# Optimization experiments

Hardware: AMD Instinct MI355X
Metric: run time of the kernel (lower is better)

Reference implementation:

```python
import jax, jax.numpy as jnp
import numpy as np

H, W, WS = 48, 48, 8          # spatial grid and window radius
D, NUM_HEADS = 256, 8          # embed dim, heads
N = H * W
K = (2 * WS + 1) ** 2          # max neighbors = 289
EPS = 1e-5


def _precompute_neighbors(h, w, ws):
    """Faithful port of SCAM._precompute_neighbors (pads ragged rows with n[0])."""
    neighbors_list = []
    for idx in range(h * w):
        row, col = idx // w, idx % w
        nb = []
        for i in range(-ws, ws + 1):
            for j in range(-ws, ws + 1):
                r, c = row + i, col + j
                if 0 <= r < h and 0 <= c < w:
                    nb.append(r * w + c)
        neighbors_list.append(nb)
    max_n = max(len(n) for n in neighbors_list)
    padded = np.array([n + [n[0]] * (max_n - len(n)) for n in neighbors_list], dtype=np.int32)
    return padded


def setup_inputs() -> dict:
    key = jax.random.key(0)
    k1, k2, k3, k4 = jax.random.split(key, 4)
    B = 1
    scale = 0.02
    return {
        "x1": jax.random.normal(k1, (B, N, D), dtype=jnp.float32),
        "x2": jax.random.normal(k2, (B, N, D), dtype=jnp.float32),
        "ln_gamma": jnp.ones((D,), jnp.float32),
        "ln_beta": jnp.zeros((D,), jnp.float32),
        "in_proj_w": jax.random.normal(k3, (3 * D, D), dtype=jnp.float32) * scale,
        "in_proj_b": jnp.zeros((3 * D,), jnp.float32),
        "out_w": jax.random.normal(k4, (D, D), dtype=jnp.float32) * scale,
        "out_b": jnp.zeros((D,), jnp.float32),
        "neighbors_idx": jnp.asarray(_precompute_neighbors(H, W, WS)),  # [N, K] int32
    }


def _layernorm(x, gamma, beta):
    mu = jnp.mean(x, axis=-1, keepdims=True)
    var = jnp.var(x, axis=-1, keepdims=True)
    return (x - mu) * jax.lax.rsqrt(var + EPS) * gamma + beta


def reference(x1, x2, ln_gamma, ln_beta, in_proj_w, in_proj_b, out_w, out_b, neighbors_idx):
    B, n, d = x1.shape
    hd = d // NUM_HEADS

    # --- neighborhood gather-attention on x2 ---
    neighbor_feats = x2[:, neighbors_idx, :]                         # [B, N, K, D]
    scores = jnp.einsum('bnd,bnkd->bnk', x2, neighbor_feats) / (d ** 0.5)
    attn_w = jax.nn.softmax(scores, axis=-1)                          # softmax over neighbors
    x2_fused = jnp.einsum('bnk,bnkd->bnd', attn_w, neighbor_feats)    # [B, N, D]
    x2_fused = _layernorm(x2_fused, ln_gamma, ln_beta)

    # --- standard MHA: query=x2_fused, key=value=x1 ---
    wq, wk, wv = in_proj_w[:d], in_proj_w[d:2 * d], in_proj_w[2 * d:]
    bq, bk, bv = in_proj_b[:d], in_proj_b[d:2 * d], in_proj_b[2 * d:]
    q = (x2_fused @ wq.T + bq).reshape(B, n, NUM_HEADS, hd).transpose(0, 2, 1, 3)
    k = (x1 @ wk.T + bk).reshape(B, n, NUM_HEADS, hd).transpose(0, 2, 1, 3)
    v = (x1 @ wv.T + bv).reshape(B, n, NUM_HEADS, hd).transpose(0, 2, 1, 3)
    logits = jnp.einsum('bhqd,bhkd->bhqk', q, k) / (hd ** 0.5)        # [B, H, N, N]
    p = jax.nn.softmax(logits, axis=-1)
    o = jnp.einsum('bhqk,bhkd->bhqd', p, v)                           # [B, H, N, hd]
    o = o.transpose(0, 2, 1, 3).reshape(B, n, d)
    return o @ out_w.T + out_b
```

## Files before the change

### kernel.cpp

```cpp
#include <hip/hip_runtime.h>
#include <math.h>

#define N 2304
#define D 256
#define K_NB 289
#define NH 8
#define HD 32
#define KS 4
#define SEG (N / KS)
#define NGR 2320

typedef __attribute__((ext_vector_type(8))) short short8;
typedef __attribute__((ext_vector_type(4))) float floatx4;

static __device__ __forceinline__ unsigned short f2bf(float x) {
  union { float f; unsigned u; } v; v.f = x;
  unsigned r = (v.u + 0x7fffu + ((v.u >> 16) & 1u)) >> 16;
  return (unsigned short)r;
}

__global__ __launch_bounds__(256) void prep_kernel(
    const float* __restrict__ x2, unsigned short* __restrict__ x2b_full,
    unsigned short* __restrict__ x2t_full)
{
  __shared__ unsigned short T[16][17];
  const int tx = threadIdx.x & 15;
  const int ty = threadIdx.x >> 4;
  const int k0 = blockIdx.x * 16;
  const int f0 = blockIdx.y * 16;
  const int key = k0 + ty - 8;
  unsigned short v = 0;
  if (key >= 0 && key < N) v = f2bf(x2[(size_t)key * D + f0 + tx]);
  x2b_full[(size_t)(k0 + ty) * D + f0 + tx] = v;
  T[ty][tx] = v;
  __syncthreads();
  x2t_full[(size_t)(f0 + ty) * NGR + k0 + tx] = T[tx][ty];
}

__global__ __launch_bounds__(256) void stage1_mfma_kernel(
    const unsigned short* __restrict__ x2b,
    const unsigned short* __restrict__ x2t,
    const float* __restrict__ gamma, const float* __restrict__ beta,
    float* __restrict__ x2f)
{
  __shared__ float S[16][548];
  __shared__ __align__(16) unsigned short Pb[16][552];
  __shared__ float dinv[16];
  __shared__ float lr1[4][16], lr2[4][16];

  const int t    = threadIdx.x;
  const int w    = t >> 6;
  const int lane = t & 63;
  const int g    = lane >> 4;
  const int cL   = lane & 15;
  const int b  = blockIdx.x;
  const int r  = b / 3;
  const int c0 = (b % 3) * 16;
  const int qbase = r * 48 + c0;
  const int row_lo = max(0, 8 - r);
  const int row_hi = min(16, 55 - r);

  short8 qf[8];
  {
    const unsigned short* qptr = x2b + (size_t)(qbase + cL) * D + g * 8;
    #pragma unroll
    for (int s = 0; s < 8; ++s) qf[s] = *(const short8*)(qptr + s * 32);
  }

  for (int wr = row_lo + w; wr <= row_hi; wr += 4) {
    const int kr = r - 8 + wr;
    const int keybase = kr * 48 + c0 - 8;
    #pragma unroll
    for (int ch = 0; ch < 2; ++ch) {
      const unsigned short* kptr = x2b + (size_t)(keybase + ch * 16 + cL) * D + g * 8;
      floatx4 sa = {0.f, 0.f, 0.f, 0.f};
      #pragma unroll
      for (int s = 0; s < 8; ++s) {
        const short8 kf = *(const short8*)(kptr + s * 32);
        sa = __builtin_amdgcn_mfma_f32_16x16x32_bf16(qf[s], kf, sa, 0, 0, 0);
      }
      #pragma unroll
      for (int reg = 0; reg < 4; ++reg)
        S[g * 4 + reg][wr * 32 + ch * 16 + cL] = sa[reg] * 0.0625f;
    }
  }
  __syncthreads();

  if (t < 16) {
    const int c = c0 + t;
    const int nrows = min(r + 8, 47) - max(r - 8, 0) + 1;
    const int ncols = min(c + 8, 47) - max(c - 8, 0) + 1;
    const int mult  = K_NB - nrows * ncols + 1;
    if (mult > 1) {
      const int wr0 = max(0, 8 - r);
      const int wc0 = (c >= 8) ? t : (8 - c0);
      S[t][wr0 * 32 + wc0] += __logf((float)mult);
    }
  }
  __syncthreads();

  {
    const int qi = t >> 4, ti = t & 15;
    float ssum = 0.f;
    for (int wk = ti; wk < 544; wk += 16) {
      const int wr = wk >> 5, wc = wk & 31;
      const int kr = r - 8 + wr;
      const int kc = c0 - 8 + wc;
      const bool valid = (kr >= 0) & (kr < 48) & (kc >= 0) & (kc < 48) &
                         (wc >= qi) & (wc <= qi + 16);
      const float p = valid ? __expf(S[qi][wk]) : 0.f;
      ssum += p;
      Pb[qi][wk] = valid ? f2bf(p) : (unsigned short)0;
    }
    #pragma unroll
    for (int off = 1; off <= 8; off <<= 1) ssum += __shfl_xor(ssum, off);
    if (ti == 0) dinv[qi] = 1.f / ssum;
  }
  __syncthreads();

  floatx4 acc[4];
  #pragma unroll
  for (int ng = 0; ng < 4; ++ng) acc[ng] = (floatx4){0.f, 0.f, 0.f, 0.f};
  const int fb = w * 64;
  for (int wr = row_lo; wr <= row_hi; ++wr) {
    const int keybase = (r - 8 + wr) * 48 + c0 - 8;
    const short8 pA = *(const short8*)&Pb[cL][wr * 32 + g * 8];
    #pragma unroll
    for (int ng = 0; ng < 4; ++ng) {
      const short8 vf = *(const short8*)(x2t + (size_t)(fb + ng * 16 + cL) * NGR + keybase + g * 8);
      acc[ng] = __builtin_amdgcn_mfma_f32_16x16x32_bf16(pA, vf, acc[ng], 0, 0, 0);
    }
  }

  float vout[4][4], ps1[4] = {0,0,0,0}, ps2[4] = {0,0,0,0};
  #pragma unroll
  for (int reg = 0; reg < 4; ++reg) {
    const float di = dinv[g * 4 + reg];
    #pragma unroll
    for (int ng = 0; ng < 4; ++ng) {
      const float v = acc[ng][reg] * di;
      vout[ng][reg] = v;
      ps1[reg] += v;
      ps2[reg] += v * v;
    }
  }
  #pragma unroll
  for (int off = 1; off <= 8; off <<= 1) {
    #pragma unroll
    for (int reg = 0; reg < 4; ++reg) {
      ps1[reg] += __shfl_xor(ps1[reg], off);
      ps2[reg] += __shfl_xor(ps2[reg], off);
    }
  }
  if (cL == 0) {
    #pragma unroll
    for (int reg = 0; reg < 4; ++reg) {
      lr1[w][g * 4 + reg] = ps1[reg];
      lr2[w][g * 4 + reg] = ps2[reg];
    }
  }
  __syncthreads();
  #pragma unroll
  for (int reg = 0; reg < 4; ++reg) {
    const int m = g * 4 + reg;
    const float s1 = lr1[0][m] + lr1[1][m] + lr1[2][m] + lr1[3][m];
    const float s2 = lr2[0][m] + lr2[1][m] + lr2[2][m] + lr2[3][m];
    const float mu  = s1 * (1.f / 256.f);
    const float var = s2 * (1.f / 256.f) - mu * mu;
    const float rs  = rsqrtf(var + 1e-5f);
    #pragma unroll
    for (int ng = 0; ng < 4; ++ng) {
      const int f = fb + ng * 16 + cL;
      x2f[(size_t)(qbase + m) * D + f] = (vout[ng][reg] - mu) * rs * gamma[f] + beta[f];
    }
  }
}

__global__ __launch_bounds__(256) void gemm_qkv_kernel(
    const float* __restrict__ A0, const float* __restrict__ A1,
    const float* __restrict__ W, const float* __restrict__ bias,
    unsigned short* __restrict__ Qb, unsigned short* __restrict__ Kb,
    unsigned short* __restrict__ Vtb)
{
  __shared__ float As[64][68];
  __shared__ float Ws[64][68];
  const int t  = threadIdx.x;
  const int tx = t & 15;
  const int ty = t >> 4;
  const int j0 = blockIdx.x * 64;
  const int m0 = blockIdx.y * 64;
  const float* __restrict__ Asrc = (j0 < 256) ? A0 : A1;

  float acc[4][4];
  #pragma unroll
  for (int r = 0; r < 4; ++r)
    #pragma unroll
    for (int c = 0; c < 4; ++c) acc[r][c] = 0.f;

  for (int kc = 0; kc < D; kc += 64) {
    const int col = tx * 4;
    #pragma unroll
    for (int i = 0; i < 4; ++i) {
      const int r = ty + 16 * i;
      *(float4*)&As[r][col] = *(const float4*)(Asrc + (size_t)(m0 + r) * D + kc + col);
      *(float4*)&Ws[r][col] = *(const float4*)(W    + (size_t)(j0 + r) * D + kc + col);
    }
    __syncthreads();
    #pragma unroll 4
    for (int kk = 0; kk < 64; kk += 4) {
      float4 a4[4], b4[4];
      #pragma unroll
      for (int r = 0; r < 4; ++r) a4[r] = *(const float4*)&As[ty * 4 + r][kk];
      #pragma unroll
      for (int c = 0; c < 4; ++c) b4[c] = *(const float4*)&Ws[tx + 16 * c][kk];
      #pragma unroll
      for (int r = 0; r < 4; ++r)
        #pragma unroll
        for (int c = 0; c < 4; ++c) {
          acc[r][c] += a4[r].x * b4[c].x;
          acc[r][c] += a4[r].y * b4[c].y;
          acc[r][c] += a4[r].z * b4[c].z;
          acc[r][c] += a4[r].w * b4[c].w;
        }
    }
    __syncthreads();
  }
  const float qscale = 0.17677669529663687f;
  #pragma unroll
  for (int r = 0; r < 4; ++r) {
    const int m = m0 + ty * 4 + r;
    #pragma unroll
    for (int c = 0; c < 4; ++c) {
      const int j = j0 + tx + 16 * c;
      const float v = acc[r][c] + bias[j];
      if (j0 < 256)       Qb[(size_t)m * D + j] = f2bf(v * qscale);
      else if (j0 < 512)  Kb[(size_t)m * D + (j - 256)] = f2bf(v);
      else                Vtb[(size_t)(j - 512) * N + m] = f2bf(v);
    }
  }
}

__global__ __launch_bounds__(256) void attn_mfma_kernel(
    const unsigned short* __restrict__ Qb, const unsigned short* __restrict__ Kb,
    const unsigned short* __restrict__ Vtb,
    float* __restrict__ pacc, float* __restrict__ psum)
{
  __shared__ __align__(16) unsigned short Pt[4][16][32];
  const int wv   = threadIdx.x >> 6;
  const int lane = threadIdx.x & 63;
  const int g    = lane >> 4;
  const int c    = lane & 15;
  const int seg  = blockIdx.x;
  const int head = blockIdx.z;
  const int qt   = blockIdx.y * 4 + wv;
  const int q0   = qt * 16;

  const short8 qf = *(const short8*)(Qb + (size_t)(q0 + c) * D + head * HD + g * 8);

  floatx4 acc0 = {0.f, 0.f, 0.f, 0.f};
  floatx4 acc1 = {0.f, 0.f, 0.f, 0.f};
  float sacc[4] = {0.f, 0.f, 0.f, 0.f};

  const int key0 = seg * SEG;
  const unsigned short* kb = Kb + (size_t)key0 * D + head * HD + g * 8;
  const unsigned short* vb = Vtb + (size_t)(head * HD + c) * N + key0 + g * 8;

  for (int kc = 0; kc < SEG; kc += 32) {
    const short8 kf0 = *(const short8*)(kb + (size_t)(kc + c) * D);
    const short8 kf1 = *(const short8*)(kb + (size_t)(kc + 16 + c) * D);
    const floatx4 z = {0.f, 0.f, 0.f, 0.f};
    floatx4 sA = __builtin_amdgcn_mfma_f32_16x16x32_bf16(qf, kf0, z, 0, 0, 0);
    floatx4 sB = __builtin_amdgcn_mfma_f32_16x16x32_bf16(qf, kf1, z, 0, 0, 0);
    #pragma unroll
    for (int r = 0; r < 4; ++r) {
      const float pa = __expf(sA[r]);
      const float pb = __expf(sB[r]);
      sacc[r] += pa + pb;
      Pt[wv][g * 4 + r][c]      = f2bf(pa);
      Pt[wv][g * 4 + r][c + 16] = f2bf(pb);
    }
    const short8 pA  = *(const short8*)&Pt[wv][c][g * 8];
    const short8 vf0 = *(const short8*)(vb + kc);
    const short8 vf1 = *(const short8*)(vb + (size_t)16 * N + kc);
    acc0 = __builtin_amdgcn_mfma_f32_16x16x32_bf16(pA, vf0, acc0, 0, 0, 0);
    acc1 = __builtin_amdgcn_mfma_f32_16x16x32_bf16(pA, vf1, acc1, 0, 0, 0);
  }

  #pragma unroll
  for (int off = 1; off <= 8; off <<= 1) {
    #pragma unroll
    for (int r = 0; r < 4; ++r) sacc[r] += __shfl_xor(sacc[r], off);
  }

  const size_t base = (size_t)(seg * NH + head) * N + q0;
  #pragma unroll
  for (int r = 0; r < 4; ++r) {
    const size_t row = base + g * 4 + r;
    pacc[row * HD + c]      = acc0[r];
    pacc[row * HD + c + 16] = acc1[r];
    if (c == 0) psum[row] = sacc[r];
  }
}

__global__ __launch_bounds__(256) void combine_kernel(
    const float* __restrict__ pacc, const float* __restrict__ psum,
    float* __restrict__ o)
{
  const int n = blockIdx.x;
  const int t = threadIdx.x;
  const int h = t >> 5;
  const int d = t & 31;
  float num = 0.f, den = 0.f;
  #pragma unroll
  for (int sgi = 0; sgi < KS; ++sgi) {
    const size_t b = (size_t)(sgi * NH + h) * N + n;
    num += pacc[b * HD + d];
    den += psum[b];
  }
  o[(size_t)n * D + t] = num / den;
}

__global__ __launch_bounds__(256) void gemm_kernel(
    const float* __restrict__ A, const float* __restrict__ W,
    const float* __restrict__ bias, float* __restrict__ C)
{
  __shared__ float As[64][68];
  __shared__ float Ws[64][68];
  const int t  = threadIdx.x;
  const int tx = t & 15;
  const int ty = t >> 4;
  const int j0 = blockIdx.x * 64;
  const int m0 = blockIdx.y * 64;

  float acc[4][4];
  #pragma unroll
  for (int r = 0; r < 4; ++r)
    #pragma unroll
    for (int c = 0; c < 4; ++c) acc[r][c] = 0.f;

  for (int kc = 0; kc < D; kc += 64) {
    const int col = tx * 4;
    #pragma unroll
    for (int i = 0; i < 4; ++i) {
      const int r = ty + 16 * i;
      *(float4*)&As[r][col] = *(const float4*)(A + (size_t)(m0 + r) * D + kc + col);
      *(float4*)&Ws[r][col] = *(const float4*)(W + (size_t)(j0 + r) * D + kc + col);
    }
    __syncthreads();
    #pragma unroll 4
    for (int kk = 0; kk < 64; kk += 4) {
      float4 a4[4], b4[4];
      #pragma unroll
      for (int r = 0; r < 4; ++r) a4[r] = *(const float4*)&As[ty * 4 + r][kk];
      #pragma unroll
      for (int c = 0; c < 4; ++c) b4[c] = *(const float4*)&Ws[tx + 16 * c][kk];
      #pragma unroll
      for (int r = 0; r < 4; ++r)
        #pragma unroll
        for (int c = 0; c < 4; ++c) {
          acc[r][c] += a4[r].x * b4[c].x;
          acc[r][c] += a4[r].y * b4[c].y;
          acc[r][c] += a4[r].z * b4[c].z;
          acc[r][c] += a4[r].w * b4[c].w;
        }
    }
    __syncthreads();
  }
  #pragma unroll
  for (int r = 0; r < 4; ++r) {
    const int m = m0 + ty * 4 + r;
    #pragma unroll
    for (int c = 0; c < 4; ++c) {
      const int j = j0 + tx + 16 * c;
      C[(size_t)m * D + j] = acc[r][c] + bias[j];
    }
  }
}

extern "C" void kernel_launch(void* const* d_in, const int* in_sizes, int n_in,
                              void* d_out, int out_size, void* d_ws, size_t ws_size,
                              hipStream_t stream)
{
  (void)in_sizes; (void)n_in; (void)out_size; (void)ws_size;
  const float* x1  = (const float*)d_in[0];
  const float* x2  = (const float*)d_in[1];
  const float* lng = (const float*)d_in[2];
  const float* lnb = (const float*)d_in[3];
  const float* ipw = (const float*)d_in[4];
  const float* ipb = (const float*)d_in[5];
  const float* ow  = (const float*)d_in[6];
  const float* ob  = (const float*)d_in[7];
  float* out = (float*)d_out;

  char* p = (char*)d_ws;
  float* x2f  = (float*)p; p += (size_t)N * D * 4;
  float* o    = (float*)p; p += (size_t)N * D * 4;
  float* pacc = (float*)p; p += (size_t)KS * NH * N * HD * 4;
  float* psum = (float*)p; p += (size_t)KS * NH * N * 4;
  unsigned short* Qb  = (unsigned short*)p; p += (size_t)N * D * 2;
  unsigned short* Kb  = (unsigned short*)p; p += (size_t)N * D * 2;
  unsigned short* Vtb = (unsigned short*)p; p += (size_t)D * N * 2;
  unsigned short* x2b_full = (unsigned short*)p; p += (size_t)NGR * D * 2;
  unsigned short* x2t_full = (unsigned short*)p; p += (size_t)D * NGR * 2;
  const unsigned short* x2b = x2b_full + (size_t)8 * D;
  const unsigned short* x2t = x2t_full + 8;

  prep_kernel<<<dim3(NGR / 16, 16), 256, 0, stream>>>(x2, x2b_full, x2t_full);
  stage1_mfma_kernel<<<144, 256, 0, stream>>>(x2b, x2t, lng, lnb, x2f);
  gemm_qkv_kernel<<<dim3(12, 36), 256, 0, stream>>>(x2f, x1, ipw, ipb, Qb, Kb, Vtb);
  attn_mfma_kernel<<<dim3(KS, 36, NH), 256, 0, stream>>>(Qb, Kb, Vtb, pacc, psum);
  combine_kernel<<<N, 256, 0, stream>>>(pacc, psum, o);
  gemm_kernel<<<dim3(4, 36), 256, 0, stream>>>(o, ow, ob, out);
}
```

Baseline: 183.1 us.

## Transpose attention MFMAs, shuffle P in registers, prefetch K/V, double key split

The attention kernel now computes S^T and O^T by swapping MFMA operand order, so the exponentiated probabilities can be repacked into the B-operand layout with cross-lane shuffles instead of a round trip through shared memory. K and V fragments for the next key chunk are loaded one iteration ahead to hide global load latency. The key-split count doubles to raise grid parallelism, and outputs are stored as float4. The trade-off is more partial results for the combine kernel to read and extra shuffle instructions per iteration.

```diff
diff --git a/kernel.cpp b/kernel.cpp
--- a/kernel.cpp
+++ b/kernel.cpp
@@ -6,7 +6,7 @@
 #define K_NB 289
 #define NH 8
 #define HD 32
-#define KS 4
+#define KS 8
 #define SEG (N / KS)
 #define NGR 2320
 
@@ -17,6 +17,9 @@
   union { float f; unsigned u; } v; v.f = x;
   unsigned r = (v.u + 0x7fffu + ((v.u >> 16) & 1u)) >> 16;
   return (unsigned short)r;
+}
+static __device__ __forceinline__ unsigned pack2bf(float lo, float hi) {
+  return (unsigned)f2bf(lo) | ((unsigned)f2bf(hi) << 16);
 }
 
 __global__ __launch_bounds__(256) void prep_kernel(
@@ -245,61 +248,81 @@
     const unsigned short* __restrict__ Vtb,
     float* __restrict__ pacc, float* __restrict__ psum)
 {
-  __shared__ __align__(16) unsigned short Pt[4][16][32];
   const int wv   = threadIdx.x >> 6;
   const int lane = threadIdx.x & 63;
   const int g    = lane >> 4;
   const int c    = lane & 15;
   const int seg  = blockIdx.x;
   const int head = blockIdx.z;
-  const int qt   = blockIdx.y * 4 + wv;
-  const int q0   = qt * 16;
+  const int q0   = (blockIdx.y * 4 + wv) * 16;
 
   const short8 qf = *(const short8*)(Qb + (size_t)(q0 + c) * D + head * HD + g * 8);
 
-  floatx4 acc0 = {0.f, 0.f, 0.f, 0.f};
-  floatx4 acc1 = {0.f, 0.f, 0.f, 0.f};
-  float sacc[4] = {0.f, 0.f, 0.f, 0.f};
+  floatx4 accL = {0.f, 0.f, 0.f, 0.f};
+  floatx4 accH = {0.f, 0.f, 0.f, 0.f};
+  float ssum = 0.f;
 
   const int key0 = seg * SEG;
-  const unsigned short* kb = Kb + (size_t)key0 * D + head * HD + g * 8;
-  const unsigned short* vb = Vtb + (size_t)(head * HD + c) * N + key0 + g * 8;
+  const unsigned short* kb  = Kb  + (size_t)key0 * D + head * HD + g * 8;
+  const unsigned short* vlo = Vtb + (size_t)(head * HD + c) * N + key0 + g * 8;
+  const unsigned short* vhi = vlo + (size_t)16 * N;
+
+  const int la = ((2 * g) & 3) * 16 + c;
+  const int lb = ((2 * g + 1) & 3) * 16 + c;
+  const bool hiHalf = (g >= 2);
+
+  short8 kf0 = *(const short8*)(kb + (size_t)c * D);
+  short8 kf1 = *(const short8*)(kb + (size_t)(16 + c) * D);
+  short8 vl  = *(const short8*)vlo;
+  short8 vh  = *(const short8*)vhi;
 
   for (int kc = 0; kc < SEG; kc += 32) {
-    const short8 kf0 = *(const short8*)(kb + (size_t)(kc + c) * D);
-    const short8 kf1 = *(const short8*)(kb + (size_t)(kc + 16 + c) * D);
+    const int nk = (kc + 32 < SEG) ? kc + 32 : 0;
+    short8 nkf0 = *(const short8*)(kb + (size_t)(nk + c) * D);
+    short8 nkf1 = *(const short8*)(kb + (size_t)(nk + 16 + c) * D);
+    short8 nvl  = *(const short8*)(vlo + nk);
+    short8 nvh  = *(const short8*)(vhi + nk);
+
     const floatx4 z = {0.f, 0.f, 0.f, 0.f};
-    floatx4 sA = __builtin_amdgcn_mfma_f32_16x16x32_bf16(qf, kf0, z, 0, 0, 0);
-    floatx4 sB = __builtin_amdgcn_mfma_f32_16x16x32_bf16(qf, kf1, z, 0, 0, 0);
+    floatx4 sA = __builtin_amdgcn_mfma_f32_16x16x32_bf16(kf0, qf, z, 0, 0, 0);
+    floatx4 sB = __builtin_amdgcn_mfma_f32_16x16x32_bf16(kf1, qf, z, 0, 0, 0);
+
+    float pa[4], pb[4];
     #pragma unroll
     for (int r = 0; r < 4; ++r) {
-      const float pa = __expf(sA[r]);
-      const float pb = __expf(sB[r]);
-      sacc[r] += pa + pb;
-      Pt[wv][g * 4 + r][c]      = f2bf(pa);
-      Pt[wv][g * 4 + r][c + 16] = f2bf(pb);
-    }
-    const short8 pA  = *(const short8*)&Pt[wv][c][g * 8];
-    const short8 vf0 = *(const short8*)(vb + kc);
-    const short8 vf1 = *(const short8*)(vb + (size_t)16 * N + kc);
-    acc0 = __builtin_amdgcn_mfma_f32_16x16x32_bf16(pA, vf0, acc0, 0, 0, 0);
-    acc1 = __builtin_amdgcn_mfma_f32_16x16x32_bf16(pA, vf1, acc1, 0, 0, 0);
-  }
-
-  #pragma unroll
-  for (int off = 1; off <= 8; off <<= 1) {
-    #pragma unroll
-    for (int r = 0; r < 4; ++r) sacc[r] += __shfl_xor(sacc[r], off);
-  }
-
-  const size_t base = (size_t)(seg * NH + head) * N + q0;
-  #pragma unroll
-  for (int r = 0; r < 4; ++r) {
-    const size_t row = base + g * 4 + r;
-    pacc[row * HD + c]      = acc0[r];
-    pacc[row * HD + c + 16] = acc1[r];
-    if (c == 0) psum[row] = sacc[r];
-  }
+      pa[r] = __expf(sA[r]);
+      pb[r] = __expf(sB[r]);
+      ssum += pa[r] + pb[r];
+    }
+    const unsigned pk0 = pack2bf(pa[0], pa[1]);
+    const unsigned pk1 = pack2bf(pa[2], pa[3]);
+    const unsigned pk2 = pack2bf(pb[0], pb[1]);
+    const unsigned pk3 = pack2bf(pb[2], pb[3]);
+    const unsigned a0 = __shfl((int)pk0, la), a1 = __shfl((int)pk1, la);
+    const unsigned b0 = __shfl((int)pk2, la), b1 = __shfl((int)pk3, la);
+    const unsigned c0 = __shfl((int)pk0, lb), c1 = __shfl((int)pk1, lb);
+    const unsigned d0 = __shfl((int)pk2, lb), d1 = __shfl((int)pk3, lb);
+    union { unsigned u[4]; short8 s; } pf;
+    pf.u[0] = hiHalf ? b0 : a0;
+    pf.u[1] = hiHalf ? b1 : a1;
+    pf.u[2] = hiHalf ? d0 : c0;
+    pf.u[3] = hiHalf ? d1 : c1;
+
+    accL = __builtin_amdgcn_mfma_f32_16x16x32_bf16(vl, pf.s, accL, 0, 0, 0);
+    accH = __builtin_amdgcn_mfma_f32_16x16x32_bf16(vh, pf.s, accH, 0, 0, 0);
+
+    kf0 = nkf0; kf1 = nkf1; vl = nvl; vh = nvh;
+  }
+
+  ssum += __shfl_xor(ssum, 16);
+  ssum += __shfl_xor(ssum, 32);
+
+  const size_t row = (size_t)(seg * NH + head) * N + q0 + c;
+  float4 o0 = make_float4(accL[0], accL[1], accL[2], accL[3]);
+  float4 o1 = make_float4(accH[0], accH[1], accH[2], accH[3]);
+  *(float4*)(pacc + row * HD + g * 4)      = o0;
+  *(float4*)(pacc + row * HD + 16 + g * 4) = o1;
+  if (g == 0) psum[row] = ssum;
 }
 
 __global__ __launch_bounds__(256) void combine_kernel(
```

After: 189.5 us. 1.04x slower.

## Restructure attention kernel with LDS double-buffered K/V and register-resident probabilities

Applied to the files above, without the earlier changes.

The attention kernel now stages K and V chunks in shared memory with double buffering, prefetching the next chunk from global memory while the current one is computed. Each wave processes four query tiles against every shared K/V chunk, so each K/V load is reused across more queries. Scores are computed transposed, which lets exp(P) be packed straight into registers as the operand of a 16x16x16 MFMA instead of making a round trip through LDS. The key split doubles from 4 to 8 segments and blocks shrink to 128 threads, which raises the partial-result traffic handled by the combine kernel and enlarges the pacc workspace.

```diff
diff --git a/kernel.cpp b/kernel.cpp
--- a/kernel.cpp
+++ b/kernel.cpp
@@ -6,17 +6,21 @@
 #define K_NB 289
 #define NH 8
 #define HD 32
-#define KS 4
+#define KS 8
 #define SEG (N / KS)
 #define NGR 2320
 
 typedef __attribute__((ext_vector_type(8))) short short8;
+typedef __attribute__((ext_vector_type(4))) short bf16x4;
 typedef __attribute__((ext_vector_type(4))) float floatx4;
 
 static __device__ __forceinline__ unsigned short f2bf(float x) {
   union { float f; unsigned u; } v; v.f = x;
   unsigned r = (v.u + 0x7fffu + ((v.u >> 16) & 1u)) >> 16;
   return (unsigned short)r;
+}
+static __device__ __forceinline__ unsigned pack2bf(float lo, float hi) {
+  return (unsigned)f2bf(lo) | ((unsigned)f2bf(hi) << 16);
 }
 
 __global__ __launch_bounds__(256) void prep_kernel(
@@ -240,65 +244,101 @@
   }
 }
 
-__global__ __launch_bounds__(256) void attn_mfma_kernel(
+__global__ __launch_bounds__(128) void attn_mfma_kernel(
     const unsigned short* __restrict__ Qb, const unsigned short* __restrict__ Kb,
     const unsigned short* __restrict__ Vtb,
     float* __restrict__ pacc, float* __restrict__ psum)
 {
-  __shared__ __align__(16) unsigned short Pt[4][16][32];
-  const int wv   = threadIdx.x >> 6;
-  const int lane = threadIdx.x & 63;
+  __shared__ __align__(16) unsigned short Ksh[2][32 * 40];
+  __shared__ __align__(16) unsigned short Vsh[2][32 * 40];
+
+  const int t    = threadIdx.x;
+  const int wv   = t >> 6;
+  const int lane = t & 63;
   const int g    = lane >> 4;
   const int c    = lane & 15;
   const int seg  = blockIdx.x;
+  const int qb   = blockIdx.y;
   const int head = blockIdx.z;
-  const int qt   = blockIdx.y * 4 + wv;
-  const int q0   = qt * 16;
-
-  const short8 qf = *(const short8*)(Qb + (size_t)(q0 + c) * D + head * HD + g * 8);
-
-  floatx4 acc0 = {0.f, 0.f, 0.f, 0.f};
-  floatx4 acc1 = {0.f, 0.f, 0.f, 0.f};
-  float sacc[4] = {0.f, 0.f, 0.f, 0.f};
-
+  const int q0w  = qb * 128 + wv * 64;
   const int key0 = seg * SEG;
-  const unsigned short* kb = Kb + (size_t)key0 * D + head * HD + g * 8;
-  const unsigned short* vb = Vtb + (size_t)(head * HD + c) * N + key0 + g * 8;
-
-  for (int kc = 0; kc < SEG; kc += 32) {
-    const short8 kf0 = *(const short8*)(kb + (size_t)(kc + c) * D);
-    const short8 kf1 = *(const short8*)(kb + (size_t)(kc + 16 + c) * D);
-    const floatx4 z = {0.f, 0.f, 0.f, 0.f};
-    floatx4 sA = __builtin_amdgcn_mfma_f32_16x16x32_bf16(qf, kf0, z, 0, 0, 0);
-    floatx4 sB = __builtin_amdgcn_mfma_f32_16x16x32_bf16(qf, kf1, z, 0, 0, 0);
-    #pragma unroll
-    for (int r = 0; r < 4; ++r) {
-      const float pa = __expf(sA[r]);
-      const float pb = __expf(sB[r]);
-      sacc[r] += pa + pb;
-      Pt[wv][g * 4 + r][c]      = f2bf(pa);
-      Pt[wv][g * 4 + r][c + 16] = f2bf(pb);
-    }
-    const short8 pA  = *(const short8*)&Pt[wv][c][g * 8];
-    const short8 vf0 = *(const short8*)(vb + kc);
-    const short8 vf1 = *(const short8*)(vb + (size_t)16 * N + kc);
-    acc0 = __builtin_amdgcn_mfma_f32_16x16x32_bf16(pA, vf0, acc0, 0, 0, 0);
-    acc1 = __builtin_amdgcn_mfma_f32_16x16x32_bf16(pA, vf1, acc1, 0, 0, 0);
-  }
-
-  #pragma unroll
-  for (int off = 1; off <= 8; off <<= 1) {
-    #pragma unroll
-    for (int r = 0; r < 4; ++r) sacc[r] += __shfl_xor(sacc[r], off);
-  }
-
-  const size_t base = (size_t)(seg * NH + head) * N + q0;
-  #pragma unroll
-  for (int r = 0; r < 4; ++r) {
-    const size_t row = base + g * 4 + r;
-    pacc[row * HD + c]      = acc0[r];
-    pacc[row * HD + c + 16] = acc1[r];
-    if (c == 0) psum[row] = sacc[r];
+
+  short8 qf[4];
+  #pragma unroll
+  for (int qt = 0; qt < 4; ++qt)
+    qf[qt] = *(const short8*)(Qb + (size_t)(q0w + qt * 16 + c) * D + head * HD + g * 8);
+
+  const unsigned short* ksrc = Kb  + (size_t)(key0 + t / 4) * D + head * HD + (t % 4) * 8;
+  const unsigned short* vsrc = Vtb + (size_t)(head * HD + t / 4) * N + key0 + (t % 4) * 8;
+  const int sdst = (t / 4) * 40 + (t % 4) * 8;
+
+  {
+    const float4 gk = *(const float4*)ksrc;
+    const float4 gv = *(const float4*)vsrc;
+    *(float4*)&Ksh[0][sdst] = gk;
+    *(float4*)&Vsh[0][sdst] = gv;
+  }
+  __syncthreads();
+
+  floatx4 accL[4], accH[4];
+  float ssum[4];
+  #pragma unroll
+  for (int qt = 0; qt < 4; ++qt) {
+    accL[qt] = (floatx4){0.f, 0.f, 0.f, 0.f};
+    accH[qt] = (floatx4){0.f, 0.f, 0.f, 0.f};
+    ssum[qt] = 0.f;
+  }
+
+  const int NCH = SEG / 32;
+  for (int ch = 0; ch < NCH; ++ch) {
+    float4 gk, gv;
+    const bool more = (ch + 1 < NCH);
+    if (more) {
+      gk = *(const float4*)(ksrc + (size_t)(ch + 1) * 32 * D);
+      gv = *(const float4*)(vsrc + (ch + 1) * 32);
+    }
+    const unsigned short* kb = Ksh[ch & 1];
+    const unsigned short* vb = Vsh[ch & 1];
+
+    #pragma unroll
+    for (int kk = 0; kk < 2; ++kk) {
+      const short8 kf  = *(const short8*)&kb[(kk * 16 + c) * 40 + g * 8];
+      const bf16x4 vf0 = *(const bf16x4*)&vb[c * 40 + kk * 16 + g * 4];
+      const bf16x4 vf1 = *(const bf16x4*)&vb[(16 + c) * 40 + kk * 16 + g * 4];
+      #pragma unroll
+      for (int qt = 0; qt < 4; ++qt) {
+        const floatx4 z = {0.f, 0.f, 0.f, 0.f};
+        floatx4 sA = __builtin_amdgcn_mfma_f32_16x16x32_bf16(kf, qf[qt], z, 0, 0, 0);
+        const float p0 = __expf(sA[0]);
+        const float p1 = __expf(sA[1]);
+        const float p2 = __expf(sA[2]);
+        const float p3 = __expf(sA[3]);
+        ssum[qt] += (p0 + p1) + (p2 + p3);
+        union { unsigned u[2]; bf16x4 s; } pB;
+        pB.u[0] = pack2bf(p0, p1);
+        pB.u[1] = pack2bf(p2, p3);
+        accL[qt] = __builtin_amdgcn_mfma_f32_16x16x16bf16_1k(vf0, pB.s, accL[qt], 0, 0, 0);
+        accH[qt] = __builtin_amdgcn_mfma_f32_16x16x16bf16_1k(vf1, pB.s, accH[qt], 0, 0, 0);
+      }
+    }
+    if (more) {
+      *(float4*)&Ksh[(ch + 1) & 1][sdst] = gk;
+      *(float4*)&Vsh[(ch + 1) & 1][sdst] = gv;
+    }
+    __syncthreads();
+  }
+
+  #pragma unroll
+  for (int qt = 0; qt < 4; ++qt) {
+    float s = ssum[qt];
+    s += __shfl_xor(s, 16);
+    s += __shfl_xor(s, 32);
+    const size_t row = (size_t)(seg * NH + head) * N + q0w + qt * 16 + c;
+    *(float4*)(pacc + row * HD + g * 4) =
+        make_float4(accL[qt][0], accL[qt][1], accL[qt][2], accL[qt][3]);
+    *(float4*)(pacc + row * HD + 16 + g * 4) =
+        make_float4(accH[qt][0], accH[qt][1], accH[qt][2], accH[qt][3]);
+    if (g == 0) psum[row] = s;
   }
 }
 
@@ -408,7 +448,7 @@
   prep_kernel<<<dim3(NGR / 16, 16), 256, 0, stream>>>(x2, x2b_full, x2t_full);
   stage1_mfma_kernel<<<144, 256, 0, stream>>>(x2b, x2t, lng, lnb, x2f);
   gemm_qkv_kernel<<<dim3(12, 36), 256, 0, stream>>>(x2f, x1, ipw, ipb, Qb, Kb, Vtb);
-  attn_mfma_kernel<<<dim3(KS, 36, NH), 256, 0, stream>>>(Qb, Kb, Vtb, pacc, psum);
+  attn_mfma_kernel<<<dim3(KS, N / 128, NH), 128, 0, stream>>>(Qb, Kb, Vtb, pacc, psum);
   combine_kernel<<<N, 256, 0, stream>>>(pacc, psum, o);
   gemm_kernel<<<dim3(4, 36), 256, 0, stream>>>(o, ow, ob, out);
 }
```

New measurement: 165.6 us. 9.6% less time.
